# Optimization experiments

Measured on AMD Instinct MI355X. Metric: run time of the kernel, lower is better.

The kernel has to match this reference:

```python
import jax, jax.numpy as jnp
import numpy as np

N_NODES = 100000
N_EDGES = 3200000


def gcn_conv(x, edge_index, W, b, n_nodes):
    # PyG GCNConv: x' = D^{-1/2} (A + I) D^{-1/2} (x W) + b
    h = x @ W  # [N, C_out]
    loop = jnp.arange(n_nodes, dtype=edge_index.dtype)
    src = jnp.concatenate([edge_index[0], loop])  # source nodes j
    dst = jnp.concatenate([edge_index[1], loop])  # target nodes i (aggregation)
    deg = jax.ops.segment_sum(jnp.ones_like(dst, h.dtype), dst, num_segments=n_nodes)
    dinv = jnp.where(deg > 0, jax.lax.rsqrt(deg), 0.0)
    norm = dinv[src] * dinv[dst]  # [E+N]
    msg = h[src] * norm[:, None]  # gather + scale
    out = jax.ops.segment_sum(msg, dst, num_segments=n_nodes)  # scatter-add
    return out + b


def setup_inputs() -> dict:
    key = jax.random.key(0)
    ks = jax.random.split(key, 6)
    x = jax.random.normal(ks[0], (N_NODES, 1), dtype=jnp.float32)
    edge_index = jax.random.randint(ks[1], (2, N_EDGES), 0, N_NODES, dtype=jnp.int64)
    W1 = jax.random.normal(ks[2], (1, 16), dtype=jnp.float32) * (1.0 / np.sqrt(1))
    b1 = jnp.zeros((16,), dtype=jnp.float32)
    W2 = jax.random.normal(ks[3], (16, 16), dtype=jnp.float32) * (1.0 / np.sqrt(16))
    b2 = jnp.zeros((16,), dtype=jnp.float32)
    Wl = jax.random.normal(ks[4], (16, 1), dtype=jnp.float32) * (1.0 / np.sqrt(16))
    bl = jnp.zeros((1,), dtype=jnp.float32)
    return {"x": x, "edge_index": edge_index, "W1": W1, "b1": b1,
            "W2": W2, "b2": b2, "Wl": Wl, "bl": bl}


def reference(x, edge_index, W1, b1, W2, b2, Wl, bl):
    n = x.shape[0]
    h = gcn_conv(x, edge_index, W1, b1, n)
    h = jax.nn.relu(h)
    # F.dropout(training=self.training): identity in eval mode
    h = gcn_conv(h, edge_index, W2, b2, n)
    return h @ Wl + bl  # [N, 1]
```

## Files before the change

### kernel.cpp

```cpp
#include <hip/hip_runtime.h>

#define N_NODES  100000
#define N_EDGES  3200000
#define NB       8
#define BN       12544
#define BNH      (BN / 2)
#define NRT      256
#define THR      1024
#define QPB      (N_EDGES / NRT / 4)
#define CAP      2048
#define SA       64
#define SPS      (NRT / SA)
#define GA       (NB * SA)
#define TRD      256
#define M17      0x1FFFFu


__global__ __launch_bounds__(THR) void k_route(
        const int* __restrict__ ei, unsigned* __restrict__ cnt,
        unsigned* __restrict__ pedge) {
    __shared__ __align__(16) unsigned stag[BN];
    __shared__ unsigned bcnt[NB], bbase[NB], bcur[NB];
    const int tid = threadIdx.x, blk = blockIdx.x;
    if (tid < NB) bcnt[tid] = 0u;
    __syncthreads();

    const uint4* s4 = (const uint4*)ei;
    const uint4* d4 = (const uint4*)(ei + N_EDGES);
    const int q0 = blk * QPB;
    uint4 dq[4], sq[4];
    #pragma unroll
    for (int i = 0; i < 4; ++i) {
        const int q = tid + i * THR;
        if (q < QPB) { dq[i] = d4[q0 + q]; sq[i] = s4[q0 + q]; }
    }

    unsigned c01 = 0, c23 = 0;
    #pragma unroll
    for (int i = 0; i < 4; ++i) {
        const int q = tid + i * THR;
        if (q < QPB) {
            const unsigned dd[4] = { dq[i].x, dq[i].y, dq[i].z, dq[i].w };
            #pragma unroll
            for (int k = 0; k < 4; ++k) {
                const unsigned b = dd[k] / BN;
                if (b < 4) c01 += 1u << (8 * b);
                else       c23 += 1u << (8 * (b - 4));
            }
        }
    }
    #pragma unroll
    for (int b = 0; b < 4; ++b) {
        const unsigned v0 = (c01 >> (8 * b)) & 0xFFu;
        const unsigned v1 = (c23 >> (8 * b)) & 0xFFu;
        if (v0) atomicAdd(&bcnt[b], v0);
        if (v1) atomicAdd(&bcnt[b + 4], v1);
    }
    __syncthreads();
    if (tid == 0) {
        unsigned run = 0;
        #pragma unroll
        for (int b = 0; b < NB; ++b) { bbase[b] = run; bcur[b] = run; run += bcnt[b]; }
    }
    __syncthreads();

    #pragma unroll
    for (int i = 0; i < 4; ++i) {
        const int q = tid + i * THR;
        if (q < QPB) {
            const unsigned dd[4] = { dq[i].x, dq[i].y, dq[i].z, dq[i].w };
            const unsigned ss[4] = { sq[i].x, sq[i].y, sq[i].z, sq[i].w };
            #pragma unroll
            for (int k = 0; k < 4; ++k) {
                const unsigned d = dd[k];
                const unsigned b = d / BN;
                const unsigned slot = atomicAdd(&bcur[b], 1u);
                stag[slot] = ss[k] | ((d - b * BN) << 17);
            }
        }
    }
    __syncthreads();

    #pragma unroll
    for (int b = 0; b < NB; ++b) {
        const unsigned n = bcnt[b] < CAP ? bcnt[b] : CAP;
        const unsigned base = bbase[b];
        unsigned* reg = pedge + ((size_t)(blk * NB + b)) * CAP;
        for (unsigned j = tid; j < n; j += THR) reg[j] = stag[base + j];
    }
    if (tid < NB) cnt[blk * NB + tid] = bcnt[tid] < CAP ? bcnt[tid] : CAP;
}

__global__ __launch_bounds__(THR, 8) void k_accd(
        const unsigned* __restrict__ pedge, const unsigned* __restrict__ cnt,
        unsigned* __restrict__ pdeg) {
    __shared__ __align__(16) unsigned ucnt[BN];
    const int tid = threadIdx.x;
    const int bu = blockIdx.x >> 6, sub = blockIdx.x & 63;
    for (int i = tid; i < BN; i += THR) ucnt[i] = 0u;
    __syncthreads();
    #pragma unroll
    for (int p = 0; p < SPS / 2; ++p) {
        const int r0 = (sub * SPS + 2 * p)     * NB + bu;
        const int r1 = (sub * SPS + 2 * p + 1) * NB + bu;
        const unsigned n0 = cnt[r0], n1 = cnt[r1];
        const uint4* g0 = (const uint4*)(pedge + (size_t)r0 * CAP);
        const uint4* g1 = (const uint4*)(pedge + (size_t)r1 * CAP);
        const unsigned q0 = n0 >> 2, q1 = n1 >> 2;
        const unsigned m4 = q0 > q1 ? q0 : q1;
        for (unsigned j = tid; j < m4; j += THR) {
            if (j < q0) {
                const uint4 w = g0[j];
                atomicAdd(&ucnt[w.x >> 17], 1u); atomicAdd(&ucnt[w.y >> 17], 1u);
                atomicAdd(&ucnt[w.z >> 17], 1u); atomicAdd(&ucnt[w.w >> 17], 1u);
            }
            if (j < q1) {
                const uint4 w = g1[j];
                atomicAdd(&ucnt[w.x >> 17], 1u); atomicAdd(&ucnt[w.y >> 17], 1u);
                atomicAdd(&ucnt[w.z >> 17], 1u); atomicAdd(&ucnt[w.w >> 17], 1u);
            }
        }
        const unsigned* e0 = (const unsigned*)g0;
        for (unsigned j = (n0 & ~3u) + tid; j < n0; j += THR)
            atomicAdd(&ucnt[e0[j] >> 17], 1u);
        const unsigned* e1 = (const unsigned*)g1;
        for (unsigned j = (n1 & ~3u) + tid; j < n1; j += THR)
            atomicAdd(&ucnt[e1[j] >> 17], 1u);
    }
    __syncthreads();
    unsigned* po = pdeg + (size_t)blockIdx.x * BNH;
    for (int i = tid; i < BNH; i += THR)
        po[i] = (ucnt[2 * i] & 0xFFFFu) | (ucnt[2 * i + 1] << 16);
}

__global__ __launch_bounds__(THR, 8) void k_acc(
        const unsigned* __restrict__ pedge, const unsigned* __restrict__ cnt,
        const float* __restrict__ vals, float* __restrict__ partials) {
    __shared__ __align__(16) float facc[BN];
    const int tid = threadIdx.x;
    const int bu = blockIdx.x >> 6, sub = blockIdx.x & 63;
    for (int i = tid; i < BN / 4; i += THR)
        ((float4*)facc)[i] = make_float4(0.f, 0.f, 0.f, 0.f);
    __syncthreads();
    #pragma unroll
    for (int p = 0; p < SPS / 2; ++p) {
        const int r0 = (sub * SPS + 2 * p)     * NB + bu;
        const int r1 = (sub * SPS + 2 * p + 1) * NB + bu;
        const unsigned n0 = cnt[r0], n1 = cnt[r1];
        const uint4* g0 = (const uint4*)(pedge + (size_t)r0 * CAP);
        const uint4* g1 = (const uint4*)(pedge + (size_t)r1 * CAP);
        const unsigned q0 = n0 >> 2, q1 = n1 >> 2;
        const unsigned m4 = q0 > q1 ? q0 : q1;
        for (unsigned j = tid; j < m4; j += THR) {
            const bool a0 = j < q0, a1 = j < q1;
            uint4 w0, w1;
            if (a0) w0 = g0[j];
            if (a1) w1 = g1[j];
            float v00, v01, v02, v03, v10, v11, v12, v13;
            if (a0) { v00 = vals[w0.x & M17]; v01 = vals[w0.y & M17];
                      v02 = vals[w0.z & M17]; v03 = vals[w0.w & M17]; }
            if (a1) { v10 = vals[w1.x & M17]; v11 = vals[w1.y & M17];
                      v12 = vals[w1.z & M17]; v13 = vals[w1.w & M17]; }
            if (a0) { atomicAdd(&facc[w0.x >> 17], v00); atomicAdd(&facc[w0.y >> 17], v01);
                      atomicAdd(&facc[w0.z >> 17], v02); atomicAdd(&facc[w0.w >> 17], v03); }
            if (a1) { atomicAdd(&facc[w1.x >> 17], v10); atomicAdd(&facc[w1.y >> 17], v11);
                      atomicAdd(&facc[w1.z >> 17], v12); atomicAdd(&facc[w1.w >> 17], v13); }
        }
        const unsigned* e0 = (const unsigned*)g0;
        for (unsigned j = (n0 & ~3u) + tid; j < n0; j += THR)
            atomicAdd(&facc[e0[j] >> 17], vals[e0[j] & M17]);
        const unsigned* e1 = (const unsigned*)g1;
        for (unsigned j = (n1 & ~3u) + tid; j < n1; j += THR)
            atomicAdd(&facc[e1[j] >> 17], vals[e1[j] & M17]);
    }
    __syncthreads();
    float4* po = (float4*)(partials + (size_t)blockIdx.x * BN);
    const float4* fi = (const float4*)facc;
    for (int i = tid; i < BN / 4; i += THR) po[i] = fi[i];
}

__device__ __forceinline__ float sum_partials(const float* __restrict__ partials,
                                              int g) {
    const int bu = g / BN, l = g - bu * BN;
    const float* pp = partials + (size_t)(bu * SA) * BN + l;
    float s = 0.f;
    #pragma unroll 16
    for (int k = 0; k < SA; ++k) s += pp[(size_t)k * BN];
    return s;
}

__global__ __launch_bounds__(TRD) void k_red1(const float* __restrict__ x,
        const unsigned* __restrict__ pdeg,
        float* __restrict__ dinv, float* __restrict__ xs) {
    const int t = blockIdx.x * TRD + threadIdx.x;
    const int g0 = 2 * t;
    if (g0 >= N_NODES) return;
    const int bu = g0 / BN, l = g0 - bu * BN;
    const unsigned* pp = pdeg + (size_t)(bu * SA) * BNH + (l >> 1);
    unsigned r0 = 0, r1 = 0;
    #pragma unroll 16
    for (int s = 0; s < SA; ++s) {
        const unsigned w = pp[(size_t)s * BNH];
        r0 += w & 0xFFFFu; r1 += w >> 16;
    }
    const float di0 = rsqrtf((float)r0 + 1.f);
    const float di1 = rsqrtf((float)r1 + 1.f);
    const float2 xv = *(const float2*)(x + g0);
    *(float2*)(dinv + g0) = make_float2(di0, di1);
    *(float2*)(xs + g0)   = make_float2(xv.x * di0, xv.y * di1);
}

__global__ __launch_bounds__(TRD) void k_red2(const float* __restrict__ x,
        const float* __restrict__ partials, const float* __restrict__ dinv,
        const float* __restrict__ W1, const float* __restrict__ b1,
        const float* __restrict__ W2, const float* __restrict__ Wl,
        float* __restrict__ us, float* __restrict__ uself) {
    const int g = blockIdx.x * TRD + threadIdx.x;
    if (g >= N_NODES) return;
    const float sum = sum_partials(partials, g);
    const float di = dinv[g];
    const float s1 = di * sum + x[g] * di * di;
    float u = 0.f;
    #pragma unroll
    for (int c = 0; c < 16; ++c) {
        float vcc = 0.f;
        #pragma unroll
        for (int k = 0; k < 16; ++k) vcc += W2[c * 16 + k] * Wl[k];
        u += fmaxf(W1[c] * s1 + b1[c], 0.f) * vcc;
    }
    us[g] = u * di;
    uself[g] = u * di * di;
}

__global__ __launch_bounds__(TRD) void k_red3(const float* __restrict__ partials,
        const float* __restrict__ dinv, const float* __restrict__ uself,
        const float* __restrict__ W2, const float* __restrict__ b2,
        const float* __restrict__ Wl, const float* __restrict__ bl,
        float* __restrict__ out) {
    const int g = blockIdx.x * TRD + threadIdx.x;
    if (g >= N_NODES) return;
    const float sum = sum_partials(partials, g);
    float vcb = bl[0];
    #pragma unroll
    for (int c = 0; c < 16; ++c) {
        float vcc = 0.f;
        #pragma unroll
        for (int k = 0; k < 16; ++k) vcc += W2[c * 16 + k] * Wl[k];
        vcb += b2[c] * vcc;
    }
    out[g] = dinv[g] * sum + uself[g] + vcb;
}

extern "C" void kernel_launch(void* const* d_in, const int* in_sizes, int n_in,
                              void* d_out, int out_size, void* d_ws, size_t ws_size,
                              hipStream_t stream) {
    const float* x  = (const float*)d_in[0];
    const int*   ei = (const int*)d_in[1];
    const float* W1 = (const float*)d_in[2];
    const float* b1 = (const float*)d_in[3];
    const float* W2 = (const float*)d_in[4];
    const float* b2 = (const float*)d_in[5];
    const float* Wl = (const float*)d_in[6];
    const float* bl = (const float*)d_in[7];
    float* out = (float*)d_out;

    unsigned* cnt      = (unsigned*)d_ws;
    unsigned* pedge    = cnt + NRT * NB;
    float*    partials = (float*)(pedge + (size_t)NRT * NB * CAP);
    unsigned* pdeg     = (unsigned*)partials;
    float*    dinv     = partials + (size_t)GA * BN;
    float*    xs       = dinv + N_NODES;
    float*    us       = xs + N_NODES;
    float*    uself    = us + N_NODES;

    const int rb1 = (N_NODES / 2 + TRD - 1) / TRD;
    const int rb  = (N_NODES + TRD - 1) / TRD;

    k_route<<<NRT, THR, 0, stream>>>(ei, cnt, pedge);
    k_accd <<<GA,  THR, 0, stream>>>(pedge, cnt, pdeg);
    k_red1 <<<rb1, TRD, 0, stream>>>(x, pdeg, dinv, xs);
    k_acc  <<<GA,  THR, 0, stream>>>(pedge, cnt, xs, partials);
    k_red2 <<<rb,  TRD, 0, stream>>>(x, partials, dinv, W1, b1, W2, Wl, us, uself);
    k_acc  <<<GA,  THR, 0, stream>>>(pedge, cnt, us, partials);
    k_red3 <<<rb,  TRD, 0, stream>>>(partials, dinv, uself, W2, b2, Wl, bl, out);
}
```

Measured before the change: 190.8 us.

## Fuse degree counting into routing kernel using byte-packed shared histograms

Removes the separate degree-accumulation pass over routed edges. Extra blocks in the routing kernel now count destination degrees directly from edge_index, using 8-bit packed counters in shared memory over two node halves. The accumulation kernels switch to 32 sub-slices instead of 64, and red1 sums 64 packed partials per group of four nodes. The byte counters risk overflow if any node receives 255 or more edges within one slice, and the dst array is now read twice.

```diff
diff --git a/kernel.cpp b/kernel.cpp
--- a/kernel.cpp
+++ b/kernel.cpp
@@ -2,31 +2,60 @@
 
 #define N_NODES  100000
 #define N_EDGES  3200000
+#define NQ       (N_EDGES / 4)
 #define NB       8
 #define BN       12544
-#define BNH      (BN / 2)
+#define HALF     50176
+#define HWH      12544
 #define NRT      256
+#define NDG      128
+#define QPB      (NQ / NRT)
+#define QDS      (NQ / 64)
 #define THR      1024
-#define QPB      (N_EDGES / NRT / 4)
 #define CAP      2048
-#define SA       64
+#define SA       32
 #define SPS      (NRT / SA)
 #define GA       (NB * SA)
 #define TRD      256
 #define M17      0x1FFFFu
 
 
-__global__ __launch_bounds__(THR) void k_route(
+__global__ __launch_bounds__(THR) void k_route_deg(
         const int* __restrict__ ei, unsigned* __restrict__ cnt,
-        unsigned* __restrict__ pedge) {
-    __shared__ __align__(16) unsigned stag[BN];
+        unsigned* __restrict__ pedge, unsigned* __restrict__ pdeg) {
+    __shared__ __align__(16) unsigned smem[HWH];
     __shared__ unsigned bcnt[NB], bbase[NB], bcur[NB];
-    const int tid = threadIdx.x, blk = blockIdx.x;
+    const int tid = threadIdx.x;
+    const uint4* d4 = (const uint4*)(ei + N_EDGES);
+
+    if (blockIdx.x >= NRT) {
+        const int idx = blockIdx.x - NRT;
+        const unsigned base = (unsigned)(idx >> 6) * HALF;
+        const int sl = idx & 63;
+        for (int i = tid; i < HWH; i += THR) smem[i] = 0u;
+        __syncthreads();
+        const int qb = sl * QDS, qe = qb + QDS;
+        for (int q = qb + tid; q < qe; q += THR) {
+            const uint4 dv = d4[q];
+            const unsigned d0 = dv.x - base, d1 = dv.y - base;
+            const unsigned d2 = dv.z - base, d3 = dv.w - base;
+            if (d0 < HALF) atomicAdd(&smem[d0 >> 2], 1u << ((d0 & 3u) << 3));
+            if (d1 < HALF) atomicAdd(&smem[d1 >> 2], 1u << ((d1 & 3u) << 3));
+            if (d2 < HALF) atomicAdd(&smem[d2 >> 2], 1u << ((d2 & 3u) << 3));
+            if (d3 < HALF) atomicAdd(&smem[d3 >> 2], 1u << ((d3 & 3u) << 3));
+        }
+        __syncthreads();
+        uint4* po = (uint4*)(pdeg + (size_t)idx * HWH);
+        const uint4* fi = (const uint4*)smem;
+        for (int i = tid; i < HWH / 4; i += THR) po[i] = fi[i];
+        return;
+    }
+
+    const int blk = blockIdx.x;
     if (tid < NB) bcnt[tid] = 0u;
     __syncthreads();
 
     const uint4* s4 = (const uint4*)ei;
-    const uint4* d4 = (const uint4*)(ei + N_EDGES);
     const int q0 = blk * QPB;
     uint4 dq[4], sq[4];
     #pragma unroll
@@ -75,7 +104,7 @@
                 const unsigned d = dd[k];
                 const unsigned b = d / BN;
                 const unsigned slot = atomicAdd(&bcur[b], 1u);
-                stag[slot] = ss[k] | ((d - b * BN) << 17);
+                smem[slot] = ss[k] | ((d - b * BN) << 17);
             }
         }
     }
@@ -86,59 +115,17 @@
         const unsigned n = bcnt[b] < CAP ? bcnt[b] : CAP;
         const unsigned base = bbase[b];
         unsigned* reg = pedge + ((size_t)(blk * NB + b)) * CAP;
-        for (unsigned j = tid; j < n; j += THR) reg[j] = stag[base + j];
+        for (unsigned j = tid; j < n; j += THR) reg[j] = smem[base + j];
     }
     if (tid < NB) cnt[blk * NB + tid] = bcnt[tid] < CAP ? bcnt[tid] : CAP;
 }
 
-__global__ __launch_bounds__(THR, 8) void k_accd(
-        const unsigned* __restrict__ pedge, const unsigned* __restrict__ cnt,
-        unsigned* __restrict__ pdeg) {
-    __shared__ __align__(16) unsigned ucnt[BN];
-    const int tid = threadIdx.x;
-    const int bu = blockIdx.x >> 6, sub = blockIdx.x & 63;
-    for (int i = tid; i < BN; i += THR) ucnt[i] = 0u;
-    __syncthreads();
-    #pragma unroll
-    for (int p = 0; p < SPS / 2; ++p) {
-        const int r0 = (sub * SPS + 2 * p)     * NB + bu;
-        const int r1 = (sub * SPS + 2 * p + 1) * NB + bu;
-        const unsigned n0 = cnt[r0], n1 = cnt[r1];
-        const uint4* g0 = (const uint4*)(pedge + (size_t)r0 * CAP);
-        const uint4* g1 = (const uint4*)(pedge + (size_t)r1 * CAP);
-        const unsigned q0 = n0 >> 2, q1 = n1 >> 2;
-        const unsigned m4 = q0 > q1 ? q0 : q1;
-        for (unsigned j = tid; j < m4; j += THR) {
-            if (j < q0) {
-                const uint4 w = g0[j];
-                atomicAdd(&ucnt[w.x >> 17], 1u); atomicAdd(&ucnt[w.y >> 17], 1u);
-                atomicAdd(&ucnt[w.z >> 17], 1u); atomicAdd(&ucnt[w.w >> 17], 1u);
-            }
-            if (j < q1) {
-                const uint4 w = g1[j];
-                atomicAdd(&ucnt[w.x >> 17], 1u); atomicAdd(&ucnt[w.y >> 17], 1u);
-                atomicAdd(&ucnt[w.z >> 17], 1u); atomicAdd(&ucnt[w.w >> 17], 1u);
-            }
-        }
-        const unsigned* e0 = (const unsigned*)g0;
-        for (unsigned j = (n0 & ~3u) + tid; j < n0; j += THR)
-            atomicAdd(&ucnt[e0[j] >> 17], 1u);
-        const unsigned* e1 = (const unsigned*)g1;
-        for (unsigned j = (n1 & ~3u) + tid; j < n1; j += THR)
-            atomicAdd(&ucnt[e1[j] >> 17], 1u);
-    }
-    __syncthreads();
-    unsigned* po = pdeg + (size_t)blockIdx.x * BNH;
-    for (int i = tid; i < BNH; i += THR)
-        po[i] = (ucnt[2 * i] & 0xFFFFu) | (ucnt[2 * i + 1] << 16);
-}
-
-__global__ __launch_bounds__(THR, 8) void k_acc(
+__global__ __launch_bounds__(THR) void k_acc(
         const unsigned* __restrict__ pedge, const unsigned* __restrict__ cnt,
         const float* __restrict__ vals, float* __restrict__ partials) {
     __shared__ __align__(16) float facc[BN];
     const int tid = threadIdx.x;
-    const int bu = blockIdx.x >> 6, sub = blockIdx.x & 63;
+    const int bu = blockIdx.x >> 5, sub = blockIdx.x & 31;
     for (int i = tid; i < BN / 4; i += THR)
         ((float4*)facc)[i] = make_float4(0.f, 0.f, 0.f, 0.f);
     __syncthreads();
@@ -193,21 +180,22 @@
         const unsigned* __restrict__ pdeg,
         float* __restrict__ dinv, float* __restrict__ xs) {
     const int t = blockIdx.x * TRD + threadIdx.x;
-    const int g0 = 2 * t;
+    const int g0 = 4 * t;
     if (g0 >= N_NODES) return;
-    const int bu = g0 / BN, l = g0 - bu * BN;
-    const unsigned* pp = pdeg + (size_t)(bu * SA) * BNH + (l >> 1);
-    unsigned r0 = 0, r1 = 0;
+    const int h = (g0 >= HALF);
+    const int lw = (g0 - h * HALF) >> 2;
+    const unsigned* pp = pdeg + (size_t)(h * 64) * HWH + lw;
+    unsigned s = 0;
     #pragma unroll 16
-    for (int s = 0; s < SA; ++s) {
-        const unsigned w = pp[(size_t)s * BNH];
-        r0 += w & 0xFFFFu; r1 += w >> 16;
-    }
-    const float di0 = rsqrtf((float)r0 + 1.f);
-    const float di1 = rsqrtf((float)r1 + 1.f);
-    const float2 xv = *(const float2*)(x + g0);
-    *(float2*)(dinv + g0) = make_float2(di0, di1);
-    *(float2*)(xs + g0)   = make_float2(xv.x * di0, xv.y * di1);
+    for (int k = 0; k < 64; ++k) s += pp[(size_t)k * HWH];
+    const float di0 = rsqrtf((float)( s        & 0xFFu) + 1.f);
+    const float di1 = rsqrtf((float)((s >>  8) & 0xFFu) + 1.f);
+    const float di2 = rsqrtf((float)((s >> 16) & 0xFFu) + 1.f);
+    const float di3 = rsqrtf((float)( s >> 24        ) + 1.f);
+    const float4 xv = *(const float4*)(x + g0);
+    *(float4*)(dinv + g0) = make_float4(di0, di1, di2, di3);
+    *(float4*)(xs + g0)   = make_float4(xv.x * di0, xv.y * di1,
+                                        xv.z * di2, xv.w * di3);
 }
 
 __global__ __launch_bounds__(TRD) void k_red2(const float* __restrict__ x,
@@ -273,11 +261,10 @@
     float*    us       = xs + N_NODES;
     float*    uself    = us + N_NODES;
 
-    const int rb1 = (N_NODES / 2 + TRD - 1) / TRD;
+    const int rb1 = (N_NODES / 4 + TRD - 1) / TRD;
     const int rb  = (N_NODES + TRD - 1) / TRD;
 
-    k_route<<<NRT, THR, 0, stream>>>(ei, cnt, pedge);
-    k_accd <<<GA,  THR, 0, stream>>>(pedge, cnt, pdeg);
+    k_route_deg<<<NRT + NDG, THR, 0, stream>>>(ei, cnt, pedge, pdeg);
     k_red1 <<<rb1, TRD, 0, stream>>>(x, pdeg, dinv, xs);
     k_acc  <<<GA,  THR, 0, stream>>>(pedge, cnt, xs, partials);
     k_red2 <<<rb,  TRD, 0, stream>>>(x, partials, dinv, W1, b1, W2, Wl, us, uself);
```

Result: faster. 180.3 us (-5.5%).
